# Performance work log

Hardware: AMD Instinct MI355X
Metric: run time of the kernel (lower is better)

## Reference

```python
import jax, jax.numpy as jnp
import numpy as np


def setup_inputs() -> dict:
    key = jax.random.key(0)
    ks = jax.random.split(key, 20)
    B, T, D, H, FC, O = 256, 256, 256, 512, 256, 2
    s = 0.02
    inp = {
        "x": jax.random.normal(ks[0], (B, T, D), jnp.float32),
        "time": jax.random.uniform(ks[1], (B, T, 1), jnp.float32),
        "Wi_w": jax.random.normal(ks[2], (H, D), jnp.float32) * s,
        "Wi_b": jnp.zeros((H,), jnp.float32),
        "Ui_w": jax.random.normal(ks[3], (H, H), jnp.float32) * s,
        "Ui_b": jnp.zeros((H,), jnp.float32),
        "bi": jnp.zeros((H,), jnp.float32),
        "Wf_w": jax.random.normal(ks[4], (H, D), jnp.float32) * s,
        "Wf_b": jnp.zeros((H,), jnp.float32),
        "Uf_w": jax.random.normal(ks[5], (H, H), jnp.float32) * s,
        "Uf_b": jnp.zeros((H,), jnp.float32),
        "bf": jnp.ones((H,), jnp.float32),
        "Wo_w": jax.random.normal(ks[6], (H, D), jnp.float32) * s,
        "Wo_b": jnp.zeros((H,), jnp.float32),
        "Uo_w": jax.random.normal(ks[7], (H, H), jnp.float32) * s,
        "Uo_b": jnp.zeros((H,), jnp.float32),
        "bo": jnp.zeros((H,), jnp.float32),
        "Wc_w": jax.random.normal(ks[8], (H, D), jnp.float32) * s,
        "Wc_b": jnp.zeros((H,), jnp.float32),
        "Uc_w": jax.random.normal(ks[9], (H, H), jnp.float32) * s,
        "Uc_b": jnp.zeros((H,), jnp.float32),
        "bc": jnp.zeros((H,), jnp.float32),
        "Wd_w": jax.random.normal(ks[10], (H, H), jnp.float32) * s,
        "b_decomp": jnp.ones((H,), jnp.float32),
        "fc_w": jax.random.normal(ks[11], (FC, H), jnp.float32) * s,
        "fc_b": jnp.zeros((FC,), jnp.float32),
        "cls_w": jax.random.normal(ks[12], (O, FC), jnp.float32) * s,
        "cls_b": jnp.zeros((O,), jnp.float32),
    }
    return inp


def reference(x, time, Wi_w, Wi_b, Ui_w, Ui_b, bi, Wf_w, Wf_b, Uf_w, Uf_b, bf,
              Wo_w, Wo_b, Uo_w, Uo_b, bo, Wc_w, Wc_b, Uc_w, Uc_b, bc,
              Wd_w, b_decomp, fc_w, fc_b, cls_w, cls_b):
    B, T, D = x.shape
    H = Ui_w.shape[0]
    # Precompute input-side gate projections across all timesteps (batched GEMM),
    # folding both the Linear bias and the extra per-gate parameter.
    xi = jnp.einsum('btd,hd->bth', x, Wi_w) + (Wi_b + bi)
    xf = jnp.einsum('btd,hd->bth', x, Wf_w) + (Wf_b + bf)
    xo = jnp.einsum('btd,hd->bth', x, Wo_w) + (Wo_b + bo)
    xc = jnp.einsum('btd,hd->bth', x, Wc_w) + (Wc_b + bc)
    # map_elapse_time: 1 / log(t + 2.7183), shape [B, T]
    Tmap = 1.0 / jnp.log(time[:, :, 0] + 2.7183)

    def step(carry, inp):
        h, c = carry
        xi_t, xf_t, xo_t, xc_t, Tt = inp  # [B,H] x4, [B]
        # time-decayed cell decomposition
        c_st = jnp.tanh(c @ Wd_w.T + b_decomp)
        c = c - c_st + Tt[:, None] * c_st
        i_t = jax.nn.sigmoid(xi_t + h @ Ui_w.T + Ui_b)
        f_t = jax.nn.sigmoid(xf_t + h @ Uf_w.T + Uf_b)
        o_t = jax.nn.sigmoid(xo_t + h @ Uo_w.T + Uo_b)
        c_hat = jnp.tanh(xc_t + h @ Uc_w.T + Uc_b)
        c = f_t * c + i_t * c_hat
        h = o_t * jnp.tanh(c)
        return (h, c), None

    h0 = jnp.zeros((B, H), x.dtype)
    c0 = jnp.zeros((B, H), x.dtype)
    scan_in = (jnp.swapaxes(xi, 0, 1), jnp.swapaxes(xf, 0, 1),
               jnp.swapaxes(xo, 0, 1), jnp.swapaxes(xc, 0, 1),
               jnp.swapaxes(Tmap, 0, 1))
    (h_T, _), _ = jax.lax.scan(step, (h0, c0), scan_in)
    # Only the last step's classifier output is returned by the original module.
    # Dropout is identity in eval mode.
    fc_out = jax.nn.relu(h_T @ fc_w.T + fc_b)
    return fc_out @ cls_w.T + cls_b
```

## Files before the change

### kernel.cpp

```cpp
#include <hip/hip_runtime.h>


#define T_STEPS 256
#define BATCH   256
#define DIN     256
#define HID     512

typedef __attribute__((ext_vector_type(8))) __bf16 bf16x8;
typedef __attribute__((ext_vector_type(4))) float  f32x4;

#define MFMA(a,b,c) __builtin_amdgcn_mfma_f32_16x16x32_bf16((a),(b),(c),0,0,0)

#define H_S     0
#define C_S     16640
#define X_S     33280
#define WIN_S   41728
#define Z_S     109312
#define LDS_SZ  128896
#define HSTR    1040
#define XSTR    528
#define ZROW    17

struct ScanP {
  const float *x, *tim;
  const float *Wi_w,*Wi_b,*Ui_w,*Ui_b,*bi;
  const float *Wf_w,*Wf_b,*Uf_w,*Uf_b,*bf_;
  const float *Wo_w,*Wo_b,*Uo_w,*Uo_b,*bo;
  const float *Wc_w,*Wc_b,*Uc_w,*Uc_b,*bc;
  const float *Wd_w,*b_dec;
  unsigned long long *hc_buf;
  float *h_final;
  unsigned int *flags;
};

__device__ __forceinline__ float fsigm(float z){ return 1.f/(1.f + __expf(-z)); }
__device__ __forceinline__ float ftanh(float z){
  float e = __expf(-2.f*fabsf(z));
  float t = (1.f - e)/(1.f + e);
  return z < 0.f ? -t : t;
}

__device__ __forceinline__ uint4 cld16(const void* p){
  uint4 r;
  asm volatile("global_load_dwordx4 %0, %1, off sc0 sc1"
               : "=v"(r) : "v"(p) : "memory");
  return r;
}
__device__ __forceinline__ void cst8(void* p, unsigned long long v){
  asm volatile("global_store_dwordx2 %0, %1, off sc0 sc1"
               :: "v"(p), "v"(v) : "memory");
}

__device__ __forceinline__ bf16x8 wfrag8(const float* p){
  const float4* p4 = (const float4*)p;
  float4 a = p4[0], b = p4[1];
  bf16x8 r = { (__bf16)a.x,(__bf16)a.y,(__bf16)a.z,(__bf16)a.w,
               (__bf16)b.x,(__bf16)b.y,(__bf16)b.z,(__bf16)b.w };
  return r;
}
__device__ __forceinline__ void zstore(char* L, int tile, int lane, f32x4 v){
  float* p = (float*)(L + Z_S) + tile*(16*ZROW) + ((lane>>4)*4)*ZROW + (lane&15);
  p[0]=v[0]; p[ZROW]=v[1]; p[2*ZROW]=v[2]; p[3*ZROW]=v[3];
}
__device__ __forceinline__ float zread(const char* L, int tile, int r, int c){
  return ((const float*)(L + Z_S))[tile*(16*ZROW) + r*ZROW + c];
}

__global__ void __launch_bounds__(256, 1) tlstm_scan(ScanP P)
{
  __shared__ __align__(16) char L[LDS_SZ];
  const int tid  = threadIdx.x;
  const int bid  = blockIdx.x;
  const int g    = bid & 15;
  const int cs   = bid >> 4;
  const int rbase = g * 16;
  const int cbase = cs * 32;
  const int wave = tid >> 6, lane = tid & 63, lo = lane & 15, hi = lane >> 4;
  const int nt   = wave & 1;
  const int gp   = wave >> 1;
  const int g0   = gp * 2, g1 = g0 + 1;

  {
    const float* Wg = (wave == 0) ? P.Wi_w : (wave == 1) ? P.Wf_w
                    : (wave == 2) ? P.Wo_w : P.Wc_w;
    const int wc = lane >> 1, q2 = lane & 1;
    const float4* src = (const float4*)(Wg + (size_t)(cbase + wc) * DIN + q2 * 128);
    char* dst = L + WIN_S + (size_t)(wave * 32 + wc) * XSTR + q2 * 256;
#pragma unroll
    for (int j = 0; j < 16; j++){
      float4 a = src[2*j], b = src[2*j+1];
      bf16x8 o = { (__bf16)a.x,(__bf16)a.y,(__bf16)a.z,(__bf16)a.w,
                   (__bf16)b.x,(__bf16)b.y,(__bf16)b.z,(__bf16)b.w };
      *(bf16x8*)(dst + j*16) = o;
    }
  }

  bf16x8 bP[16], bQ[16], bR[16];
  {
    const float* Pw = (gp == 0) ? P.Ui_w : P.Uo_w;
    const float* Qw = (gp == 0) ? P.Uf_w : P.Uc_w;
    const size_t colb = (size_t)(cbase + nt * 16 + lo) * HID;
#pragma unroll
    for (int kc = 0; kc < 16; kc++){
      bP[kc] = wfrag8(Pw + colb + kc * 32 + hi * 8);
      bQ[kc] = wfrag8(Qw + colb + kc * 32 + hi * 8);
    }
    if (wave >= 2){
#pragma unroll
      for (int kc = 0; kc < 16; kc++)
        bR[kc] = wfrag8(P.Wd_w + colb + kc * 32 + hi * 8);
    }
  }

  const int erow = tid >> 4;
  const int ecp  = (tid & 15) * 2;
  float bias_i[2], bias_f[2], bias_o[2], bias_c[2], bias_d[2], cr[2];
#pragma unroll
  for (int e = 0; e < 2; e++){
    int c = cbase + ecp + e;
    bias_i[e] = P.Wi_b[c] + P.bi[c]  + P.Ui_b[c];
    bias_f[e] = P.Wf_b[c] + P.bf_[c] + P.Uf_b[c];
    bias_o[e] = P.Wo_b[c] + P.bo[c]  + P.Uo_b[c];
    bias_c[e] = P.Wc_b[c] + P.bc[c]  + P.Uc_b[c];
    bias_d[e] = P.b_dec[c];
    cr[e] = 0.f;
  }

  const int srow = tid >> 4, sseg = tid & 15;
  const size_t pub_off = ((size_t)(rbase + erow) * 256 + cs * 16 + (tid & 15)) * 8;

  __syncthreads();

#pragma unroll 1
  for (int t = 0; t < T_STEPS; ++t){
    const int rp = t & 1;
    const char* hcprev = (const char*)(P.hc_buf + (size_t)rp * BATCH * 256);
    char* hcnext = (char*)(P.hc_buf + (size_t)(rp ^ 1) * BATCH * 256);

    const float4* xsrc = (const float4*)(P.x + ((size_t)(rbase + srow) * T_STEPS + t) * DIN + sseg * 16);
    float4 xv[4];
#pragma unroll
    for (int j = 0; j < 4; j++) xv[j] = xsrc[j];
    float tv = P.tim[(size_t)(rbase + erow) * T_STEPS + t];

    uint4 gr[8];
    const char* src = hcprev + (size_t)(rbase + wave * 4) * 2048;
#pragma unroll
    for (int j = 0; j < 8; j++){
      int row = j >> 1;
      int gg  = (j & 1) * 64 + lane;
      gr[j] = cld16(src + (size_t)row * 2048 + (size_t)gg * 16);
    }

    {
      char* dst = L + X_S + srow * XSTR + sseg * 32;
#pragma unroll
      for (int j = 0; j < 2; j++){
        float4 a = xv[2*j], b = xv[2*j+1];
        bf16x8 o = { (__bf16)a.x,(__bf16)a.y,(__bf16)a.z,(__bf16)a.w,
                     (__bf16)b.x,(__bf16)b.y,(__bf16)b.z,(__bf16)b.w };
        *(bf16x8*)(dst + j*16) = o;
      }
    }

    asm volatile("s_waitcnt vmcnt(0)" ::: "memory");
    __builtin_amdgcn_sched_barrier(0);

    {
      const unsigned int expv = (unsigned int)(t & 1)
                              | ((unsigned int)((t >> 1) & 1) << 16);
      unsigned int stale = 0;
#pragma unroll
      for (int j = 0; j < 8; j++){
        unsigned int bad = ((gr[j].x ^ expv) | (gr[j].y ^ expv)
                          | (gr[j].z ^ expv) | (gr[j].w ^ expv)) & 0x00010001u;
        stale |= (bad ? 1u : 0u) << j;
      }
      int guard = 0;
      while (__any((int)stale) && ++guard < 65536){
#pragma unroll
        for (int j = 0; j < 8; j++){
          if (stale & (1u << j)){
            int row = j >> 1;
            int gg  = (j & 1) * 64 + lane;
            gr[j] = cld16(src + (size_t)row * 2048 + (size_t)gg * 16);
          }
        }
        asm volatile("s_waitcnt vmcnt(0)" ::: "memory");
        __builtin_amdgcn_sched_barrier(0);
        unsigned int ns = 0;
#pragma unroll
        for (int j = 0; j < 8; j++){
          if (stale & (1u << j)){
            unsigned int bad = ((gr[j].x ^ expv) | (gr[j].y ^ expv)
                              | (gr[j].z ^ expv) | (gr[j].w ^ expv)) & 0x00010001u;
            ns |= (bad ? 1u : 0u) << j;
          }
        }
        stale = ns;
      }
    }

    {
#pragma unroll
      for (int j = 0; j < 8; j++){
        int row = wave * 4 + (j >> 1);
        int gg  = (j & 1) * 64 + lane;
        *(uint2*)(L + H_S + row * HSTR + gg * 8) = uint2{gr[j].x, gr[j].z};
        *(uint2*)(L + C_S + row * HSTR + gg * 8) = uint2{gr[j].y, gr[j].w};
      }
    }
    __syncthreads();

    {
      f32x4 zA = {0.f,0.f,0.f,0.f}, zB = zA, zD = zA, xA = zA, xB = zA;
#pragma unroll
      for (int kc = 0; kc < 16; kc++){
        bf16x8 a = *(const bf16x8*)(L + H_S + lo * HSTR + kc*64 + hi*16);
        zA = MFMA(a, bP[kc], zA);
        zB = MFMA(a, bQ[kc], zB);
      }
      if (wave >= 2){
#pragma unroll
        for (int kc = 0; kc < 16; kc++){
          bf16x8 a = *(const bf16x8*)(L + C_S + lo * HSTR + kc*64 + hi*16);
          zD = MFMA(a, bR[kc], zD);
        }
      }
#pragma unroll
      for (int q = 0; q < 8; q++){
        bf16x8 ax = *(const bf16x8*)(L + X_S + lo * XSTR + q*64 + hi*16);
        bf16x8 w0 = *(const bf16x8*)(L + WIN_S + (size_t)(g0*32 + nt*16 + lo) * XSTR + q*64 + hi*16);
        bf16x8 w1 = *(const bf16x8*)(L + WIN_S + (size_t)(g1*32 + nt*16 + lo) * XSTR + q*64 + hi*16);
        xA = MFMA(ax, w0, xA);
        xB = MFMA(ax, w1, xB);
      }
      zstore(L, g0*2+nt,    lane, zA);  zstore(L, g1*2+nt,    lane, zB);
      zstore(L, 10+g0*2+nt, lane, xA);  zstore(L, 10+g1*2+nt, lane, xB);
      if (wave >= 2) zstore(L, 8+nt, lane, zD);
    }
    __syncthreads();

    {
      float Tmap = 1.f / __logf(tv + 2.7183f);
      unsigned int hpk = 0, cpk = 0;
      float hv2[2];
#pragma unroll
      for (int e = 0; e < 2; e++){
        int col = ecp + e;
        int ntc = col >> 4, cl = col & 15;
        float zi = zread(L, 0+ntc,  erow, cl) + zread(L, 10+0+ntc,  erow, cl) + bias_i[e];
        float zf = zread(L, 2+ntc,  erow, cl) + zread(L, 10+2+ntc,  erow, cl) + bias_f[e];
        float zo = zread(L, 4+ntc,  erow, cl) + zread(L, 10+4+ntc,  erow, cl) + bias_o[e];
        float zc = zread(L, 6+ntc,  erow, cl) + zread(L, 10+6+ntc,  erow, cl) + bias_c[e];
        float zdv = zread(L, 8+ntc, erow, cl) + bias_d[e];
        float cst = ftanh(zdv);
        float c1  = cr[e] - cst + Tmap * cst;
        float ig = fsigm(zi), fg = fsigm(zf), og = fsigm(zo);
        float ch = ftanh(zc);
        float c2 = fg * c1 + ig * ch;
        float hv_ = og * ftanh(c2);
        cr[e] = c2; hv2[e] = hv_;
        hpk |= (unsigned int)__builtin_bit_cast(unsigned short, (__bf16)hv_) << (16*e);
        cpk |= (unsigned int)__builtin_bit_cast(unsigned short, (__bf16)c2) << (16*e);
      }
      if (t < T_STEPS - 1){
        const unsigned int wtag  = (unsigned int)((t + 1) & 3);
        const unsigned int tmask = (wtag & 1u) | ((wtag >> 1) << 16);
        hpk = (hpk & 0xFFFEFFFEu) | tmask;
        cpk = (cpk & 0xFFFEFFFEu) | tmask;
        cst8(hcnext + pub_off,
             (unsigned long long)hpk | ((unsigned long long)cpk << 32));
      } else {
        size_t off = (size_t)(rbase + erow) * HID + cbase + ecp;
        P.h_final[off]     = hv2[0];
        P.h_final[off + 1] = hv2[1];
      }
    }
    __syncthreads();
  }
}

__global__ void __launch_bounds__(256) tlstm_head(const float* __restrict__ hfin,
    const float* __restrict__ fc_w, const float* __restrict__ fc_b,
    const float* __restrict__ cls_w, const float* __restrict__ cls_b,
    float* __restrict__ out)
{
  __shared__ float hrow[512];
  __shared__ float fcv[256];
  const int b = blockIdx.x, tid = threadIdx.x;
  ((float2*)hrow)[tid] = ((const float2*)(hfin + (size_t)b * 512))[tid];
  __syncthreads();
  {
    const float4* w4 = (const float4*)(fc_w + (size_t)tid * 512);
    const float4* h4 = (const float4*)hrow;
    float acc = fc_b[tid];
#pragma unroll 4
    for (int k = 0; k < 128; k++){
      float4 w = w4[k], h = h4[k];
      acc += w.x*h.x + w.y*h.y + w.z*h.z + w.w*h.w;
    }
    fcv[tid] = fmaxf(acc, 0.f);
  }
  __syncthreads();
  const int wave = tid >> 6, lane = tid & 63;
  if (wave < 2){
    const float* cw = cls_w + wave * 256;
    float s = 0.f;
#pragma unroll
    for (int j = lane; j < 256; j += 64) s += fcv[j] * cw[j];
#pragma unroll
    for (int off = 32; off > 0; off >>= 1) s += __shfl_down(s, off, 64);
    if (lane == 0) out[b * 2 + wave] = s + cls_b[wave];
  }
}

extern "C" void kernel_launch(void* const* d_in, const int* in_sizes, int n_in,
                              void* d_out, int out_size, void* d_ws, size_t ws_size,
                              hipStream_t stream)
{
  (void)in_sizes; (void)n_in; (void)out_size; (void)ws_size;

  ScanP P;
  P.x    = (const float*)d_in[0];
  P.tim  = (const float*)d_in[1];
  P.Wi_w = (const float*)d_in[2];  P.Wi_b = (const float*)d_in[3];
  P.Ui_w = (const float*)d_in[4];  P.Ui_b = (const float*)d_in[5];  P.bi  = (const float*)d_in[6];
  P.Wf_w = (const float*)d_in[7];  P.Wf_b = (const float*)d_in[8];
  P.Uf_w = (const float*)d_in[9];  P.Uf_b = (const float*)d_in[10]; P.bf_ = (const float*)d_in[11];
  P.Wo_w = (const float*)d_in[12]; P.Wo_b = (const float*)d_in[13];
  P.Uo_w = (const float*)d_in[14]; P.Uo_b = (const float*)d_in[15]; P.bo  = (const float*)d_in[16];
  P.Wc_w = (const float*)d_in[17]; P.Wc_b = (const float*)d_in[18];
  P.Uc_w = (const float*)d_in[19]; P.Uc_b = (const float*)d_in[20]; P.bc  = (const float*)d_in[21];
  P.Wd_w = (const float*)d_in[22]; P.b_dec = (const float*)d_in[23];
  const float* fc_w  = (const float*)d_in[24];
  const float* fc_b  = (const float*)d_in[25];
  const float* cls_w = (const float*)d_in[26];
  const float* cls_b = (const float*)d_in[27];

  unsigned long long* hc_buf = (unsigned long long*)d_ws;
  unsigned int* flags = (unsigned int*)(hc_buf + 2 * BATCH * 256);
  float* h_final = (float*)((char*)flags + 1024);
  P.hc_buf = hc_buf; P.h_final = h_final; P.flags = flags;

  const size_t zero_bytes = (size_t)2 * BATCH * 256 * 8 + 1024;
  hipMemsetAsync(d_ws, 0, zero_bytes, stream);

  hipLaunchKernelGGL(tlstm_scan, dim3(256), dim3(256), 0, stream, P);
  hipLaunchKernelGGL(tlstm_head, dim3(256), dim3(256), 0, stream,
                     h_final, fc_w, fc_b, cls_w, cls_b, (float*)d_out);
}
```

Baseline: 1.066 ms.

## Compute all four gates per wave in registers, dropping the LDS z-exchange and a barrier

Each wave now handles a 16-column tile and computes all four recurrent gate GEMMs, the decomposition GEMM and the input projections itself. The gate update then runs directly on the MFMA accumulator registers, which removes the LDS staging of pre-activations and one __syncthreads per timestep. To free registers, Wd is moved to LDS, and h/c are published as packed 32-bit words with per-element tag bits. Each wave now does more MFMA work per step (duplicated Wd and x-projection work across the two waves that share a column tile), and register pressure rises with 64 bf16x8 weight fragments held per lane.

```diff
diff --git a/kernel.cpp b/kernel.cpp
--- a/kernel.cpp
+++ b/kernel.cpp
@@ -15,11 +15,10 @@
 #define C_S     16640
 #define X_S     33280
 #define WIN_S   41728
-#define Z_S     109312
-#define LDS_SZ  128896
+#define WD_S    109312
+#define LDS_SZ  142592
 #define HSTR    1040
 #define XSTR    528
-#define ZROW    17
 
 struct ScanP {
   const float *x, *tim;
@@ -28,9 +27,8 @@
   const float *Wo_w,*Wo_b,*Uo_w,*Uo_b,*bo;
   const float *Wc_w,*Wc_b,*Uc_w,*Uc_b,*bc;
   const float *Wd_w,*b_dec;
-  unsigned long long *hc_buf;
+  unsigned int *hc_buf;
   float *h_final;
-  unsigned int *flags;
 };
 
 __device__ __forceinline__ float fsigm(float z){ return 1.f/(1.f + __expf(-z)); }
@@ -46,8 +44,8 @@
                : "=v"(r) : "v"(p) : "memory");
   return r;
 }
-__device__ __forceinline__ void cst8(void* p, unsigned long long v){
-  asm volatile("global_store_dwordx2 %0, %1, off sc0 sc1"
+__device__ __forceinline__ void cst4(void* p, unsigned int v){
+  asm volatile("global_store_dword %0, %1, off sc0 sc1"
                :: "v"(p), "v"(v) : "memory");
 }
 
@@ -57,13 +55,6 @@
   bf16x8 r = { (__bf16)a.x,(__bf16)a.y,(__bf16)a.z,(__bf16)a.w,
                (__bf16)b.x,(__bf16)b.y,(__bf16)b.z,(__bf16)b.w };
   return r;
-}
-__device__ __forceinline__ void zstore(char* L, int tile, int lane, f32x4 v){
-  float* p = (float*)(L + Z_S) + tile*(16*ZROW) + ((lane>>4)*4)*ZROW + (lane&15);
-  p[0]=v[0]; p[ZROW]=v[1]; p[2*ZROW]=v[2]; p[3*ZROW]=v[3];
-}
-__device__ __forceinline__ float zread(const char* L, int tile, int r, int c){
-  return ((const float*)(L + Z_S))[tile*(16*ZROW) + r*ZROW + c];
 }
 
 __global__ void __launch_bounds__(256, 1) tlstm_scan(ScanP P)
@@ -76,9 +67,8 @@
   const int rbase = g * 16;
   const int cbase = cs * 32;
   const int wave = tid >> 6, lane = tid & 63, lo = lane & 15, hi = lane >> 4;
-  const int nt   = wave & 1;
-  const int gp   = wave >> 1;
-  const int g0   = gp * 2, g1 = g0 + 1;
+  const int nt   = wave >> 1;
+  const int p    = wave & 1;
 
   {
     const float* Wg = (wave == 0) ? P.Wi_w : (wave == 1) ? P.Wf_w
@@ -94,62 +84,67 @@
       *(bf16x8*)(dst + j*16) = o;
     }
   }
-
-  bf16x8 bP[16], bQ[16], bR[16];
   {
-    const float* Pw = (gp == 0) ? P.Ui_w : P.Uo_w;
-    const float* Qw = (gp == 0) ? P.Uf_w : P.Uc_w;
+    const int col = tid >> 3, seg = tid & 7;
+    const float4* src = (const float4*)(P.Wd_w + (size_t)(cbase + col) * HID + seg * 64);
+    char* dst = L + WD_S + (size_t)col * 1040 + seg * 128;
+#pragma unroll
+    for (int j = 0; j < 8; j++){
+      float4 a = src[2*j], b = src[2*j+1];
+      bf16x8 o = { (__bf16)a.x,(__bf16)a.y,(__bf16)a.z,(__bf16)a.w,
+                   (__bf16)b.x,(__bf16)b.y,(__bf16)b.z,(__bf16)b.w };
+      *(bf16x8*)(dst + j*16) = o;
+    }
+  }
+
+  bf16x8 bUi[16], bUf[16], bUo[16], bUc[16];
+  {
     const size_t colb = (size_t)(cbase + nt * 16 + lo) * HID;
 #pragma unroll
     for (int kc = 0; kc < 16; kc++){
-      bP[kc] = wfrag8(Pw + colb + kc * 32 + hi * 8);
-      bQ[kc] = wfrag8(Qw + colb + kc * 32 + hi * 8);
-    }
-    if (wave >= 2){
-#pragma unroll
-      for (int kc = 0; kc < 16; kc++)
-        bR[kc] = wfrag8(P.Wd_w + colb + kc * 32 + hi * 8);
-    }
-  }
-
-  const int erow = tid >> 4;
-  const int ecp  = (tid & 15) * 2;
-  float bias_i[2], bias_f[2], bias_o[2], bias_c[2], bias_d[2], cr[2];
-#pragma unroll
-  for (int e = 0; e < 2; e++){
-    int c = cbase + ecp + e;
-    bias_i[e] = P.Wi_b[c] + P.bi[c]  + P.Ui_b[c];
-    bias_f[e] = P.Wf_b[c] + P.bf_[c] + P.Uf_b[c];
-    bias_o[e] = P.Wo_b[c] + P.bo[c]  + P.Uo_b[c];
-    bias_c[e] = P.Wc_b[c] + P.bc[c]  + P.Uc_b[c];
-    bias_d[e] = P.b_dec[c];
-    cr[e] = 0.f;
-  }
+      bUi[kc] = wfrag8(P.Ui_w + colb + kc * 32 + hi * 8);
+      bUf[kc] = wfrag8(P.Uf_w + colb + kc * 32 + hi * 8);
+      bUo[kc] = wfrag8(P.Uo_w + colb + kc * 32 + hi * 8);
+      bUc[kc] = wfrag8(P.Uc_w + colb + kc * 32 + hi * 8);
+    }
+  }
+
+  const int colg = cbase + nt * 16 + (lane & 15);
+  const int rb4  = (lane >> 4) * 4;
+  const int pub_on = ((lane >> 5) == p);
+  float Bi = P.Wi_b[colg] + P.bi[colg]  + P.Ui_b[colg];
+  float Bf = P.Wf_b[colg] + P.bf_[colg] + P.Uf_b[colg];
+  float Bo = P.Wo_b[colg] + P.bo[colg]  + P.Uo_b[colg];
+  float Bc = P.Wc_b[colg] + P.bc[colg]  + P.Uc_b[colg];
+  float Bd = P.b_dec[colg];
+  f32x4 cr = {0.f, 0.f, 0.f, 0.f};
 
   const int srow = tid >> 4, sseg = tid & 15;
-  const size_t pub_off = ((size_t)(rbase + erow) * 256 + cs * 16 + (tid & 15)) * 8;
 
   __syncthreads();
 
 #pragma unroll 1
   for (int t = 0; t < T_STEPS; ++t){
     const int rp = t & 1;
-    const char* hcprev = (const char*)(P.hc_buf + (size_t)rp * BATCH * 256);
-    char* hcnext = (char*)(P.hc_buf + (size_t)(rp ^ 1) * BATCH * 256);
+    const char* hcprevB = (const char*)(P.hc_buf + (size_t)rp * BATCH * HID);
+    char* hcnextB = (char*)(P.hc_buf + (size_t)(rp ^ 1) * BATCH * HID);
 
     const float4* xsrc = (const float4*)(P.x + ((size_t)(rbase + srow) * T_STEPS + t) * DIN + sseg * 16);
     float4 xv[4];
 #pragma unroll
     for (int j = 0; j < 4; j++) xv[j] = xsrc[j];
-    float tv = P.tim[(size_t)(rbase + erow) * T_STEPS + t];
+    float tmv[4];
+#pragma unroll
+    for (int j = 0; j < 4; j++)
+      tmv[j] = P.tim[(size_t)(rbase + rb4 + j) * T_STEPS + t];
 
     uint4 gr[8];
-    const char* src = hcprev + (size_t)(rbase + wave * 4) * 2048;
+    const char* src = hcprevB + (size_t)(rbase + wave * 4) * 2048;
 #pragma unroll
     for (int j = 0; j < 8; j++){
       int row = j >> 1;
-      int gg  = (j & 1) * 64 + lane;
-      gr[j] = cld16(src + (size_t)row * 2048 + (size_t)gg * 16);
+      int Lg  = (j & 1) * 64 + lane;
+      gr[j] = cld16(src + (size_t)row * 2048 + (size_t)Lg * 16);
     }
 
     {
@@ -167,8 +162,8 @@
     __builtin_amdgcn_sched_barrier(0);
 
     {
-      const unsigned int expv = (unsigned int)(t & 1)
-                              | ((unsigned int)((t >> 1) & 1) << 16);
+      const unsigned int expv = ((unsigned int)(t & 1) << 16)
+                              |  (unsigned int)((t >> 1) & 1);
       unsigned int stale = 0;
 #pragma unroll
       for (int j = 0; j < 8; j++){
@@ -182,8 +177,8 @@
         for (int j = 0; j < 8; j++){
           if (stale & (1u << j)){
             int row = j >> 1;
-            int gg  = (j & 1) * 64 + lane;
-            gr[j] = cld16(src + (size_t)row * 2048 + (size_t)gg * 16);
+            int Lg  = (j & 1) * 64 + lane;
+            gr[j] = cld16(src + (size_t)row * 2048 + (size_t)Lg * 16);
           }
         }
         asm volatile("s_waitcnt vmcnt(0)" ::: "memory");
@@ -205,76 +200,75 @@
 #pragma unroll
       for (int j = 0; j < 8; j++){
         int row = wave * 4 + (j >> 1);
-        int gg  = (j & 1) * 64 + lane;
-        *(uint2*)(L + H_S + row * HSTR + gg * 8) = uint2{gr[j].x, gr[j].z};
-        *(uint2*)(L + C_S + row * HSTR + gg * 8) = uint2{gr[j].y, gr[j].w};
+        int Lg  = (j & 1) * 64 + lane;
+        uint2 hp = { (gr[j].x >> 16) | (gr[j].y & 0xffff0000u),
+                     (gr[j].z >> 16) | (gr[j].w & 0xffff0000u) };
+        uint2 cp = { (gr[j].x & 0xffffu) | (gr[j].y << 16),
+                     (gr[j].z & 0xffffu) | (gr[j].w << 16) };
+        *(uint2*)(L + H_S + row * HSTR + Lg * 8) = hp;
+        *(uint2*)(L + C_S + row * HSTR + Lg * 8) = cp;
       }
     }
     __syncthreads();
 
+    f32x4 zi_ = {0.f,0.f,0.f,0.f}, zf_ = zi_, zo_ = zi_, zc_ = zi_, zd_ = zi_;
+    f32x4 xi_ = zi_, xf_ = zi_, xo_ = zi_, xc_ = zi_;
+#pragma unroll
+    for (int kc = 0; kc < 16; kc++){
+      bf16x8 a = *(const bf16x8*)(L + H_S + lo * HSTR + kc*64 + hi*16);
+      zi_ = MFMA(a, bUi[kc], zi_);
+      zf_ = MFMA(a, bUf[kc], zf_);
+      zo_ = MFMA(a, bUo[kc], zo_);
+      zc_ = MFMA(a, bUc[kc], zc_);
+    }
+#pragma unroll
+    for (int kc = 0; kc < 16; kc++){
+      bf16x8 a  = *(const bf16x8*)(L + C_S + lo * HSTR + kc*64 + hi*16);
+      bf16x8 wd = *(const bf16x8*)(L + WD_S + (size_t)(nt*16 + lo) * 1040 + kc*64 + hi*16);
+      zd_ = MFMA(a, wd, zd_);
+    }
+#pragma unroll
+    for (int q = 0; q < 8; q++){
+      bf16x8 ax = *(const bf16x8*)(L + X_S + lo * XSTR + q*64 + hi*16);
+      bf16x8 w0 = *(const bf16x8*)(L + WIN_S + (size_t)(0*32 + nt*16 + lo) * XSTR + q*64 + hi*16);
+      bf16x8 w1 = *(const bf16x8*)(L + WIN_S + (size_t)(1*32 + nt*16 + lo) * XSTR + q*64 + hi*16);
+      bf16x8 w2 = *(const bf16x8*)(L + WIN_S + (size_t)(2*32 + nt*16 + lo) * XSTR + q*64 + hi*16);
+      bf16x8 w3 = *(const bf16x8*)(L + WIN_S + (size_t)(3*32 + nt*16 + lo) * XSTR + q*64 + hi*16);
+      xi_ = MFMA(ax, w0, xi_);
+      xf_ = MFMA(ax, w1, xf_);
+      xo_ = MFMA(ax, w2, xo_);
+      xc_ = MFMA(ax, w3, xc_);
+    }
+
     {
-      f32x4 zA = {0.f,0.f,0.f,0.f}, zB = zA, zD = zA, xA = zA, xB = zA;
-#pragma unroll
-      for (int kc = 0; kc < 16; kc++){
-        bf16x8 a = *(const bf16x8*)(L + H_S + lo * HSTR + kc*64 + hi*16);
-        zA = MFMA(a, bP[kc], zA);
-        zB = MFMA(a, bQ[kc], zB);
-      }
-      if (wave >= 2){
-#pragma unroll
-        for (int kc = 0; kc < 16; kc++){
-          bf16x8 a = *(const bf16x8*)(L + C_S + lo * HSTR + kc*64 + hi*16);
-          zD = MFMA(a, bR[kc], zD);
-        }
-      }
-#pragma unroll
-      for (int q = 0; q < 8; q++){
-        bf16x8 ax = *(const bf16x8*)(L + X_S + lo * XSTR + q*64 + hi*16);
-        bf16x8 w0 = *(const bf16x8*)(L + WIN_S + (size_t)(g0*32 + nt*16 + lo) * XSTR + q*64 + hi*16);
-        bf16x8 w1 = *(const bf16x8*)(L + WIN_S + (size_t)(g1*32 + nt*16 + lo) * XSTR + q*64 + hi*16);
-        xA = MFMA(ax, w0, xA);
-        xB = MFMA(ax, w1, xB);
-      }
-      zstore(L, g0*2+nt,    lane, zA);  zstore(L, g1*2+nt,    lane, zB);
-      zstore(L, 10+g0*2+nt, lane, xA);  zstore(L, 10+g1*2+nt, lane, xB);
-      if (wave >= 2) zstore(L, 8+nt, lane, zD);
-    }
-    __syncthreads();
-
-    {
-      float Tmap = 1.f / __logf(tv + 2.7183f);
-      unsigned int hpk = 0, cpk = 0;
-      float hv2[2];
-#pragma unroll
-      for (int e = 0; e < 2; e++){
-        int col = ecp + e;
-        int ntc = col >> 4, cl = col & 15;
-        float zi = zread(L, 0+ntc,  erow, cl) + zread(L, 10+0+ntc,  erow, cl) + bias_i[e];
-        float zf = zread(L, 2+ntc,  erow, cl) + zread(L, 10+2+ntc,  erow, cl) + bias_f[e];
-        float zo = zread(L, 4+ntc,  erow, cl) + zread(L, 10+4+ntc,  erow, cl) + bias_o[e];
-        float zc = zread(L, 6+ntc,  erow, cl) + zread(L, 10+6+ntc,  erow, cl) + bias_c[e];
-        float zdv = zread(L, 8+ntc, erow, cl) + bias_d[e];
+      const unsigned int e0n = (unsigned int)((t + 1) & 1);
+      const unsigned int e1n = (unsigned int)(((t + 1) >> 1) & 1);
+#pragma unroll
+      for (int j = 0; j < 4; j++){
+        float zi = zi_[j] + xi_[j] + Bi;
+        float zf = zf_[j] + xf_[j] + Bf;
+        float zo = zo_[j] + xo_[j] + Bo;
+        float zc = zc_[j] + xc_[j] + Bc;
+        float zdv = zd_[j] + Bd;
+        float Tmap = 1.f / __logf(tmv[j] + 2.7183f);
         float cst = ftanh(zdv);
-        float c1  = cr[e] - cst + Tmap * cst;
+        float c1  = cr[j] - cst + Tmap * cst;
         float ig = fsigm(zi), fg = fsigm(zf), og = fsigm(zo);
         float ch = ftanh(zc);
         float c2 = fg * c1 + ig * ch;
-        float hv_ = og * ftanh(c2);
-        cr[e] = c2; hv2[e] = hv_;
-        hpk |= (unsigned int)__builtin_bit_cast(unsigned short, (__bf16)hv_) << (16*e);
-        cpk |= (unsigned int)__builtin_bit_cast(unsigned short, (__bf16)c2) << (16*e);
-      }
-      if (t < T_STEPS - 1){
-        const unsigned int wtag  = (unsigned int)((t + 1) & 3);
-        const unsigned int tmask = (wtag & 1u) | ((wtag >> 1) << 16);
-        hpk = (hpk & 0xFFFEFFFEu) | tmask;
-        cpk = (cpk & 0xFFFEFFFEu) | tmask;
-        cst8(hcnext + pub_off,
-             (unsigned long long)hpk | ((unsigned long long)cpk << 32));
-      } else {
-        size_t off = (size_t)(rbase + erow) * HID + cbase + ecp;
-        P.h_final[off]     = hv2[0];
-        P.h_final[off + 1] = hv2[1];
+        float hv = og * ftanh(c2);
+        cr[j] = c2;
+        if (t < T_STEPS - 1){
+          if (pub_on){
+            unsigned int hb = (unsigned int)__builtin_bit_cast(unsigned short, (__bf16)hv);
+            unsigned int cb = (unsigned int)__builtin_bit_cast(unsigned short, (__bf16)c2);
+            unsigned int w = (((hb & 0xFFFEu) | e0n) << 16)
+                           |  ((cb & 0xFFFEu) | e1n);
+            cst4(hcnextB + (size_t)(rbase + rb4 + j) * 2048 + (size_t)colg * 4, w);
+          }
+        } else if (pub_on){
+          P.h_final[(size_t)(rbase + rb4 + j) * HID + colg] = hv;
+        }
       }
     }
     __syncthreads();
@@ -338,13 +332,11 @@
   const float* cls_w = (const float*)d_in[26];
   const float* cls_b = (const float*)d_in[27];
 
-  unsigned long long* hc_buf = (unsigned long long*)d_ws;
-  unsigned int* flags = (unsigned int*)(hc_buf + 2 * BATCH * 256);
-  float* h_final = (float*)((char*)flags + 1024);
-  P.hc_buf = hc_buf; P.h_final = h_final; P.flags = flags;
-
-  const size_t zero_bytes = (size_t)2 * BATCH * 256 * 8 + 1024;
-  hipMemsetAsync(d_ws, 0, zero_bytes, stream);
+  unsigned int* hc_buf = (unsigned int*)d_ws;
+  float* h_final = (float*)(hc_buf + 2 * BATCH * HID);
+  P.hc_buf = hc_buf; P.h_final = h_final;
+
+  hipMemsetAsync(d_ws, 0, (size_t)2 * BATCH * HID * 4, stream);
 
   hipLaunchKernelGGL(tlstm_scan, dim3(256), dim3(256), 0, stream, P);
   hipLaunchKernelGGL(tlstm_head, dim3(256), dim3(256), 0, stream,
```

Result: slower. 1.459 ms (+36.9%).
